# Optimization experiments

Hardware: AMD Instinct MI355X
Metric: run time of the kernel (lower is better)

The kernel has to match this reference:

```python
import jax, jax.numpy as jnp
import numpy as np

D_MODEL, D_K, D_V, H = 1024, 64, 64, 16
NEG_INF = -1e30  # finite stand-in for -inf masked_fill (grad-safe)


def setup_inputs() -> dict:
    key = jax.random.key(0)
    ks = jax.random.split(key, 16)
    b, nq, nk = 2, 1024, 1024
    def xavier(k, fan_in, fan_out):
        lim = np.sqrt(6.0 / (fan_in + fan_out)).astype(np.float32)
        return jax.random.uniform(k, (fan_in, fan_out), jnp.float32, -lim, lim)
    return {
        "queries": jax.random.normal(ks[0], (b, nq, D_MODEL), jnp.float32),
        "keys": jax.random.normal(ks[1], (b, nk, D_MODEL), jnp.float32),
        "values": jax.random.normal(ks[2], (b, nk, D_MODEL), jnp.float32),
        "attention_mask": jax.random.randint(ks[3], (b, H, nq, nk), 0, 2, jnp.int32),
        "attention_weights": jax.random.uniform(ks[4], (b, H, nq, nk), jnp.float32),
        "Wq": xavier(ks[5], D_MODEL, H * D_K), "bq": jnp.zeros((H * D_K,), jnp.float32),
        "Wk": xavier(ks[6], D_MODEL, H * D_K), "bk": jnp.zeros((H * D_K,), jnp.float32),
        "Wv": xavier(ks[7], D_MODEL, H * D_V), "bv": jnp.zeros((H * D_V,), jnp.float32),
        "Wo": xavier(ks[8], H * D_V, D_MODEL), "bo": jnp.zeros((D_MODEL,), jnp.float32),
    }


def reference(queries, keys, values, attention_mask, attention_weights,
              Wq, bq, Wk, bk, Wv, bv, Wo, bo):
    b, nq, _ = queries.shape
    nk = keys.shape[1]
    # project and split heads: [b, h, n, d]
    Q = (queries @ Wq + bq).reshape(b, nq, H, D_K).transpose(0, 2, 1, 3)
    K = (keys @ Wk + bk).reshape(b, nk, H, D_K).transpose(0, 2, 1, 3)
    V = (values @ Wv + bv).reshape(b, nk, H, D_V).transpose(0, 2, 1, 3)
    scale = jnp.asarray(1.0 / np.sqrt(D_K), queries.dtype)
    att = jnp.einsum('bhqd,bhkd->bhqk', Q, K) * scale
    att_map = att  # pre-weight/mask scores (torch .clone())
    att = att * attention_weights            # way='mul'
    att = jnp.where(attention_mask == 0, NEG_INF, att)
    att = jax.nn.softmax(att, axis=-1)
    out = jnp.einsum('bhqk,bhkd->bqhd', att, V).reshape(b, nq, H * D_V)
    out = out @ Wo + bo
    return out, att_map
```

## Files before the change

### kernel.cpp

```cpp
#include <hip/hip_runtime.h>

typedef _Float16 f16;
typedef __attribute__((ext_vector_type(4))) _Float16 half4;
typedef __attribute__((ext_vector_type(8))) _Float16 half8;
typedef __attribute__((ext_vector_type(4))) float v4f;
typedef __attribute__((ext_vector_type(4))) float f32x4v;
typedef __attribute__((ext_vector_type(4))) int i32x4;
typedef __attribute__((ext_vector_type(8))) unsigned short u16x8;

#define NEG_BIG -1e30f

#define MFMA32(a, b, c) __builtin_amdgcn_mfma_f32_16x16x32_f16(a, b, c, 0, 0, 0)
#if __has_builtin(__builtin_amdgcn_mfma_f32_16x16x16_f16)
#define MFMA16(a, b, c) __builtin_amdgcn_mfma_f32_16x16x16_f16(a, b, c, 0, 0, 0)
#else
#define MFMA16(a, b, c) __builtin_amdgcn_mfma_f32_16x16x16f16(a, b, c, 0, 0, 0)
#endif

__global__ __launch_bounds__(256) void cvt3_kernel(
    const float* __restrict__ q, const float* __restrict__ k, const float* __restrict__ v,
    f16* __restrict__ oq, f16* __restrict__ ok, f16* __restrict__ ov)
{
    int gid = blockIdx.x * 256 + threadIdx.x;
    int seg = gid >> 19;
    int off = (gid & 524287) << 2;
    const float* src = (seg == 0) ? q : (seg == 1) ? k : v;
    f16* dst = (seg == 0) ? oq : (seg == 1) ? ok : ov;
    f32x4v x = *(const f32x4v*)(src + off);
    union { f16 h[4]; unsigned long long u; } pk;
    pk.h[0] = (f16)x[0]; pk.h[1] = (f16)x[1]; pk.h[2] = (f16)x[2]; pk.h[3] = (f16)x[3];
    *(unsigned long long*)(dst + off) = pk.u;
}

__global__ __launch_bounds__(256) void wtrans_kernel(
    const float* __restrict__ w0, const float* __restrict__ w1,
    const float* __restrict__ w2, const float* __restrict__ w3,
    f16* __restrict__ o0, f16* __restrict__ o1, f16* __restrict__ o2, f16* __restrict__ o3)
{
    __shared__ f16 tile[64][72];
    int zs = blockIdx.z;
    const float* W = (zs == 0) ? w0 : (zs == 1) ? w1 : (zs == 2) ? w2 : w3;
    f16* O = (zs == 0) ? o0 : (zs == 1) ? o1 : (zs == 2) ? o2 : o3;
    int cx = blockIdx.x * 64;
    int ry = blockIdx.y * 64;
    int tid = threadIdx.x;
    #pragma unroll
    for (int p = 0; p < 4; ++p) {
        int idx = tid + p * 256;
        int r = idx >> 4, c4 = (idx & 15) << 2;
        f32x4v x = *(const f32x4v*)&W[(size_t)(ry + r) * 1024 + cx + c4];
        tile[r][c4 + 0] = (f16)x[0]; tile[r][c4 + 1] = (f16)x[1];
        tile[r][c4 + 2] = (f16)x[2]; tile[r][c4 + 3] = (f16)x[3];
    }
    __syncthreads();
    #pragma unroll
    for (int p = 0; p < 2; ++p) {
        int idx = tid + p * 256;
        int n = idx >> 3, c8 = (idx & 7) << 3;
        union { f16 h[8]; u16x8 u; } pk;
        #pragma unroll
        for (int j = 0; j < 8; ++j) pk.h[j] = tile[c8 + j][n];
        *(u16x8*)&O[(size_t)(cx + n) * 1024 + ry + c8] = pk.u;
    }
}

__device__ __forceinline__ void gemm_core(
    const f16* __restrict__ A, const f16* __restrict__ Bt,
    const float* __restrict__ bias, void* __restrict__ out, int mode)
{
    __shared__ f16 As[128 * 72];
    __shared__ f16 Bs[64 * 72];
    const int mbase = blockIdx.y * 128;
    const int nbase = blockIdx.x * 64;
    int tid = threadIdx.x;
    int lane = tid & 63, wave = tid >> 6;
    int ln = lane & 15, hi = lane >> 4;
    int wr = wave & 1, wc = wave >> 1;
    v4f acc[4][2];
    #pragma unroll
    for (int rt = 0; rt < 4; ++rt)
        #pragma unroll
        for (int ct = 0; ct < 2; ++ct) acc[rt][ct] = (v4f){0.f, 0.f, 0.f, 0.f};

    for (int kb = 0; kb < 1024; kb += 64) {
        __syncthreads();
        #pragma unroll
        for (int p = 0; p < 4; ++p) {
            int idx = tid + p * 256;
            int r = idx >> 3, c8 = (idx & 7) << 3;
            *(u16x8*)&As[r * 72 + c8] = *(const u16x8*)&A[(size_t)(mbase + r) * 1024 + kb + c8];
        }
        #pragma unroll
        for (int p = 0; p < 2; ++p) {
            int idx = tid + p * 256;
            int r = idx >> 3, c8 = (idx & 7) << 3;
            *(u16x8*)&Bs[r * 72 + c8] = *(const u16x8*)&Bt[(size_t)(nbase + r) * 1024 + kb + c8];
        }
        __syncthreads();
        #pragma unroll
        for (int kk = 0; kk < 64; kk += 32) {
            half8 aF[4], bF[2];
            #pragma unroll
            for (int rt = 0; rt < 4; ++rt)
                aF[rt] = *(const half8*)&As[(wr * 64 + rt * 16 + ln) * 72 + kk + 8 * hi];
            #pragma unroll
            for (int ct = 0; ct < 2; ++ct)
                bF[ct] = *(const half8*)&Bs[(wc * 32 + ct * 16 + ln) * 72 + kk + 8 * hi];
            #pragma unroll
            for (int rt = 0; rt < 4; ++rt)
                #pragma unroll
                for (int ct = 0; ct < 2; ++ct)
                    acc[rt][ct] = __builtin_amdgcn_mfma_f32_16x16x32_f16(aF[rt], bF[ct], acc[rt][ct], 0, 0, 0);
        }
    }
    #pragma unroll
    for (int rt = 0; rt < 4; ++rt)
      #pragma unroll
      for (int ct = 0; ct < 2; ++ct)
        #pragma unroll
        for (int r = 0; r < 4; ++r) {
            int m = mbase + wr * 64 + rt * 16 + hi * 4 + r;
            int n = nbase + wc * 32 + ct * 16 + ln;
            float val = acc[rt][ct][r] + bias[n];
            if (mode == 0) {
                int bb = m >> 10, nq = m & 1023, hh = n >> 6, d = n & 63;
                ((f16*)out)[(((size_t)(bb * 16 + hh)) * 1024 + nq) * 64 + d] = (f16)val;
            } else if (mode == 1) {
                int bb = m >> 10, nq = m & 1023, hh = n >> 6, d = n & 63;
                ((f16*)out)[(((size_t)(bb * 16 + hh)) * 64 + d) * 1024 + nq] = (f16)val;
            } else {
                ((float*)out)[(size_t)m * 1024 + n] = val;
            }
        }
}

__global__ __launch_bounds__(256) void qkv_gemm_kernel(
    const f16* __restrict__ xq, const f16* __restrict__ xk, const f16* __restrict__ xv,
    const f16* __restrict__ wqt, const f16* __restrict__ wkt, const f16* __restrict__ wvt,
    const float* __restrict__ bq, const float* __restrict__ bk, const float* __restrict__ bv,
    f16* __restrict__ oQ, f16* __restrict__ oK, f16* __restrict__ oVt)
{
    int z = blockIdx.z;
    const f16* A  = (z == 0) ? xq  : (z == 1) ? xk  : xv;
    const f16* B  = (z == 0) ? wqt : (z == 1) ? wkt : wvt;
    const float* bi = (z == 0) ? bq : (z == 1) ? bk : bv;
    void* out = (z == 0) ? (void*)oQ : (z == 1) ? (void*)oK : (void*)oVt;
    gemm_core(A, B, bi, out, (z == 2) ? 1 : 0);
}

__global__ __launch_bounds__(256) void o_gemm_kernel(
    const f16* __restrict__ A, const f16* __restrict__ Wot,
    const float* __restrict__ bo, float* __restrict__ out)
{
    gemm_core(A, Wot, bo, out, 2);
}

__global__ __launch_bounds__(512, 2) void attn_kernel(
    const f16* __restrict__ Qp, const f16* __restrict__ Kp, const f16* __restrict__ Vt,
    const float* __restrict__ weights, const int* __restrict__ mask,
    float* __restrict__ amap, float* __restrict__ Po, float* __restrict__ Ml)
{
    __shared__ f16 Ks[512 * 72];
    __shared__ f16 Vs[64 * 520];

    int h = blockIdx.x, qc = blockIdx.y, zid = blockIdx.z;
    int b = zid >> 1, kh = zid & 1;
    int bh = b * 16 + h;
    int tid = threadIdx.x;
    int lane = tid & 63, wave = tid >> 6;
    int ln = lane & 15, hi = lane >> 4;

    const f16* Kb = Kp + ((size_t)bh * 1024 + kh * 512) * 64;
    const f16* Vb = Vt + (size_t)bh * 64 * 1024 + kh * 512;

    #pragma unroll
    for (int i = 0; i < 8; ++i) {
        int c = tid + i * 512;
        int r = c >> 3, g = c & 7;
        *(u16x8*)&Ks[r * 72 + g * 8] = *(const u16x8*)&Kb[(size_t)c * 8];
    }
    #pragma unroll
    for (int i = 0; i < 8; ++i) {
        int c = tid + i * 512;
        int r = c >> 6, g = c & 63;
        *(u16x8*)&Vs[r * 520 + g * 8] = *(const u16x8*)&Vb[(size_t)r * 1024 + g * 8];
    }

    int qg = qc * 128 + wave * 16 + ln;
    const f16*  Qb = Qp + ((size_t)bh * 1024 + qg) * 64;
    const float* Wr = weights + ((size_t)bh * 1024 + qg) * 1024 + kh * 512;
    const int*   Mr = mask    + ((size_t)bh * 1024 + qg) * 1024 + kh * 512;
    float*       Ar = amap    + ((size_t)bh * 1024 + qg) * 1024 + kh * 512;

    half8 qf0 = *(const half8*)&Qb[8 * hi];
    half8 qf1 = *(const half8*)&Qb[32 + 8 * hi];

    float mrun = -3.0e38f, lrun = 0.f;
    v4f oacc[4];
    #pragma unroll
    for (int dt = 0; dt < 4; ++dt) oacc[dt] = (v4f){0.f, 0.f, 0.f, 0.f};

    f32x4v wA[4], wB[4]; i32x4 mA[4], mB[4];
    #pragma unroll
    for (int t = 0; t < 4; ++t) {
        wA[t] = *(const f32x4v*)&Wr[t * 16 + 4 * hi];
        mA[t] = *(const i32x4*)&Mr[t * 16 + 4 * hi];
        wB[t] = *(const f32x4v*)&Wr[64 + t * 16 + 4 * hi];
        mB[t] = *(const i32x4*)&Mr[64 + t * 16 + 4 * hi];
    }
    __syncthreads();

    auto process = [&](int kt, const f32x4v (&wb)[4], const i32x4 (&mb)[4]) {
        v4f st[4];
        #pragma unroll
        for (int t = 0; t < 4; ++t) {
            const f16* kr = &Ks[(kt * 64 + t * 16 + ln) * 72 + 8 * hi];
            half8 ka = *(const half8*)kr;
            half8 kc = *(const half8*)(kr + 32);
            v4f a = (v4f){0.f, 0.f, 0.f, 0.f};
            a = MFMA32(ka, qf0, a);
            a = MFMA32(kc, qf1, a);
            st[t] = a;
        }
        float z[4][4];
        #pragma unroll
        for (int t = 0; t < 4; ++t) {
            f32x4v sv = st[t] * 0.125f;
            __builtin_nontemporal_store(sv, (f32x4v*)&Ar[kt * 64 + t * 16 + 4 * hi]);
            #pragma unroll
            for (int r = 0; r < 4; ++r)
                z[t][r] = (mb[t][r] == 0) ? NEG_BIG : sv[r] * wb[t][r];
        }
        float tm = z[0][0];
        #pragma unroll
        for (int t = 0; t < 4; ++t)
            #pragma unroll
            for (int r = 0; r < 4; ++r) tm = fmaxf(tm, z[t][r]);
        tm = fmaxf(tm, __shfl_xor(tm, 16, 64));
        tm = fmaxf(tm, __shfl_xor(tm, 32, 64));
        float mnew = fmaxf(mrun, tm);
        float fsc = __expf(mrun - mnew);
        float p[4][4];
        float tsum = 0.f;
        #pragma unroll
        for (int t = 0; t < 4; ++t)
            #pragma unroll
            for (int r = 0; r < 4; ++r) { p[t][r] = __expf(z[t][r] - mnew); tsum += p[t][r]; }
        tsum += __shfl_xor(tsum, 16, 64);
        tsum += __shfl_xor(tsum, 32, 64);
        lrun = lrun * fsc + tsum;
        mrun = mnew;
        #pragma unroll
        for (int dt = 0; dt < 4; ++dt) oacc[dt] *= fsc;
        half4 pf[4];
        #pragma unroll
        for (int t = 0; t < 4; ++t) {
            half4 v;
            v[0] = (f16)p[t][0]; v[1] = (f16)p[t][1];
            v[2] = (f16)p[t][2]; v[3] = (f16)p[t][3];
            pf[t] = v;
        }
        #pragma unroll
        for (int t = 0; t < 4; ++t)
            #pragma unroll
            for (int dt = 0; dt < 4; ++dt) {
                half4 vf = *(const half4*)&Vs[(dt * 16 + ln) * 520 + kt * 64 + t * 16 + 4 * hi];
                oacc[dt] = MFMA16(vf, pf[t], oacc[dt]);
            }
    };

    #pragma unroll 1
    for (int kt2 = 0; kt2 < 4; ++kt2) {
        int kt = kt2 * 2;
        process(kt, wA, mA);
        if (kt2 < 3) {
            #pragma unroll
            for (int t = 0; t < 4; ++t) {
                wA[t] = *(const f32x4v*)&Wr[(kt + 2) * 64 + t * 16 + 4 * hi];
                mA[t] = *(const i32x4*)&Mr[(kt + 2) * 64 + t * 16 + 4 * hi];
            }
        }
        process(kt + 1, wB, mB);
        if (kt2 < 3) {
            #pragma unroll
            for (int t = 0; t < 4; ++t) {
                wB[t] = *(const f32x4v*)&Wr[(kt + 3) * 64 + t * 16 + 4 * hi];
                mB[t] = *(const i32x4*)&Mr[(kt + 3) * 64 + t * 16 + 4 * hi];
            }
        }
    }

    size_t prow = ((size_t)kh * 32 + bh) * 1024 + qg;
    #pragma unroll
    for (int dt = 0; dt < 4; ++dt)
        *(f32x4v*)&Po[prow * 64 + dt * 16 + 4 * hi] = oacc[dt];
    if (hi == 0) {
        float2 ml = make_float2(mrun, lrun);
        *(float2*)&Ml[prow * 2] = ml;
    }
}

__global__ __launch_bounds__(256) void merge_kernel(
    const float* __restrict__ Po, const float* __restrict__ Ml, f16* __restrict__ hout)
{
    int gid = blockIdx.x * 256 + threadIdx.x;
    int dq = gid & 15;
    int q  = (gid >> 4) & 1023;
    int bh = gid >> 14;
    int b = bh >> 4, h = bh & 15;
    size_t r0 = (size_t)bh * 1024 + q;
    size_t r1 = (size_t)(32 + bh) * 1024 + q;
    float2 ml0 = *(const float2*)&Ml[r0 * 2];
    float2 ml1 = *(const float2*)&Ml[r1 * 2];
    float M = fmaxf(ml0.x, ml1.x);
    float w0 = __expf(ml0.x - M), w1 = __expf(ml1.x - M);
    float rL = 1.0f / (w0 * ml0.y + w1 * ml1.y);
    f32x4v o0 = *(const f32x4v*)&Po[r0 * 64 + dq * 4];
    f32x4v o1 = *(const f32x4v*)&Po[r1 * 64 + dq * 4];
    half4 ov;
    #pragma unroll
    for (int j = 0; j < 4; ++j) ov[j] = (f16)((w0 * o0[j] + w1 * o1[j]) * rL);
    *(half4*)&hout[((size_t)(b * 1024 + q)) * 1024 + h * 64 + dq * 4] = ov;
}

extern "C" void kernel_launch(void* const* d_in, const int* in_sizes, int n_in,
                              void* d_out, int out_size, void* d_ws, size_t ws_size,
                              hipStream_t stream)
{
    const float* queries  = (const float*)d_in[0];
    const float* keys     = (const float*)d_in[1];
    const float* values   = (const float*)d_in[2];
    const int*   amask    = (const int*)d_in[3];
    const float* aweights = (const float*)d_in[4];
    const float* Wq = (const float*)d_in[5];  const float* bq = (const float*)d_in[6];
    const float* Wk = (const float*)d_in[7];  const float* bk = (const float*)d_in[8];
    const float* Wv = (const float*)d_in[9];  const float* bv = (const float*)d_in[10];
    const float* Wo = (const float*)d_in[11]; const float* bo = (const float*)d_in[12];

    char* ws = (char*)d_ws;
    const size_t MB = 1024 * 1024;
    f16* q_h  = (f16*)(ws + 0 * MB);
    f16* k_h  = (f16*)(ws + 4 * MB);
    f16* v_h  = (f16*)(ws + 8 * MB);
    f16* wqt  = (f16*)(ws + 12 * MB);
    f16* wkt  = (f16*)(ws + 14 * MB);
    f16* wvt  = (f16*)(ws + 16 * MB);
    f16* wot  = (f16*)(ws + 18 * MB);
    f16* Qp   = (f16*)(ws + 20 * MB);
    f16* Kp   = (f16*)(ws + 24 * MB);
    f16* Vt   = (f16*)(ws + 28 * MB);
    f16* hout = (f16*)(ws + 32 * MB);
    float* Po = (float*)(ws + 0 * MB);
    float* Ml = (float*)(ws + 16 * MB);

    float* out_main = (float*)d_out;
    float* att_map  = out_main + (size_t)2 * 1024 * 1024;

    cvt3_kernel<<<6144, 256, 0, stream>>>(queries, keys, values, q_h, k_h, v_h);
    wtrans_kernel<<<dim3(16, 16, 4), 256, 0, stream>>>(Wq, Wk, Wv, Wo, wqt, wkt, wvt, wot);
    qkv_gemm_kernel<<<dim3(16, 16, 3), 256, 0, stream>>>(q_h, k_h, v_h, wqt, wkt, wvt,
                                                         bq, bk, bv, Qp, Kp, Vt);
    attn_kernel<<<dim3(16, 8, 4), 512, 0, stream>>>(Qp, Kp, Vt, aweights, amask,
                                                    att_map, Po, Ml);
    merge_kernel<<<2048, 256, 0, stream>>>(Po, Ml, hout);
    o_gemm_kernel<<<dim3(16, 16, 1), 256, 0, stream>>>(hout, wot, bo, out_main);
}
```

Baseline: 160.6 us.

## Split attention keys into four chunks and store partial outputs in fp16

The attention kernel now splits the 1024 keys into four 256-key chunks instead of two halves. This doubles the grid to 1024 blocks, halves shared memory per block and raises the occupancy hint to 4 blocks per CU. Partial outputs are written as fp16 rather than fp32 to limit the extra workspace traffic, and the merge kernel combines four partials with log-sum-exp rescaling. The cost is more partial-result traffic and a larger merge, plus some precision loss from fp16 partials.

```diff
diff --git a/kernel.cpp b/kernel.cpp
--- a/kernel.cpp
+++ b/kernel.cpp
@@ -155,42 +155,42 @@
     gemm_core(A, Wot, bo, out, 2);
 }
 
-__global__ __launch_bounds__(512, 2) void attn_kernel(
+__global__ __launch_bounds__(512, 4) void attn_kernel(
     const f16* __restrict__ Qp, const f16* __restrict__ Kp, const f16* __restrict__ Vt,
     const float* __restrict__ weights, const int* __restrict__ mask,
-    float* __restrict__ amap, float* __restrict__ Po, float* __restrict__ Ml)
-{
-    __shared__ f16 Ks[512 * 72];
-    __shared__ f16 Vs[64 * 520];
+    float* __restrict__ amap, f16* __restrict__ Po, float* __restrict__ Ml)
+{
+    __shared__ f16 Ks[256 * 72];
+    __shared__ f16 Vs[64 * 264];
 
     int h = blockIdx.x, qc = blockIdx.y, zid = blockIdx.z;
-    int b = zid >> 1, kh = zid & 1;
+    int b = zid >> 2, kq = zid & 3;
     int bh = b * 16 + h;
     int tid = threadIdx.x;
     int lane = tid & 63, wave = tid >> 6;
     int ln = lane & 15, hi = lane >> 4;
 
-    const f16* Kb = Kp + ((size_t)bh * 1024 + kh * 512) * 64;
-    const f16* Vb = Vt + (size_t)bh * 64 * 1024 + kh * 512;
-
-    #pragma unroll
-    for (int i = 0; i < 8; ++i) {
+    const f16* Kb = Kp + ((size_t)bh * 1024 + kq * 256) * 64;
+    const f16* Vb = Vt + (size_t)bh * 64 * 1024 + kq * 256;
+
+    #pragma unroll
+    for (int i = 0; i < 4; ++i) {
         int c = tid + i * 512;
         int r = c >> 3, g = c & 7;
         *(u16x8*)&Ks[r * 72 + g * 8] = *(const u16x8*)&Kb[(size_t)c * 8];
     }
     #pragma unroll
-    for (int i = 0; i < 8; ++i) {
+    for (int i = 0; i < 4; ++i) {
         int c = tid + i * 512;
-        int r = c >> 6, g = c & 63;
-        *(u16x8*)&Vs[r * 520 + g * 8] = *(const u16x8*)&Vb[(size_t)r * 1024 + g * 8];
+        int r = c >> 5, g = c & 31;
+        *(u16x8*)&Vs[r * 264 + g * 8] = *(const u16x8*)&Vb[(size_t)r * 1024 + g * 8];
     }
 
     int qg = qc * 128 + wave * 16 + ln;
     const f16*  Qb = Qp + ((size_t)bh * 1024 + qg) * 64;
-    const float* Wr = weights + ((size_t)bh * 1024 + qg) * 1024 + kh * 512;
-    const int*   Mr = mask    + ((size_t)bh * 1024 + qg) * 1024 + kh * 512;
-    float*       Ar = amap    + ((size_t)bh * 1024 + qg) * 1024 + kh * 512;
+    const float* Wr = weights + ((size_t)bh * 1024 + qg) * 1024 + kq * 256;
+    const int*   Mr = mask    + ((size_t)bh * 1024 + qg) * 1024 + kq * 256;
+    float*       Ar = amap    + ((size_t)bh * 1024 + qg) * 1024 + kq * 256;
 
     half8 qf0 = *(const half8*)&Qb[8 * hi];
     half8 qf1 = *(const half8*)&Qb[32 + 8 * hi];
@@ -264,16 +264,16 @@
         for (int t = 0; t < 4; ++t)
             #pragma unroll
             for (int dt = 0; dt < 4; ++dt) {
-                half4 vf = *(const half4*)&Vs[(dt * 16 + ln) * 520 + kt * 64 + t * 16 + 4 * hi];
+                half4 vf = *(const half4*)&Vs[(dt * 16 + ln) * 264 + kt * 64 + t * 16 + 4 * hi];
                 oacc[dt] = MFMA16(vf, pf[t], oacc[dt]);
             }
     };
 
     #pragma unroll 1
-    for (int kt2 = 0; kt2 < 4; ++kt2) {
+    for (int kt2 = 0; kt2 < 2; ++kt2) {
         int kt = kt2 * 2;
         process(kt, wA, mA);
-        if (kt2 < 3) {
+        if (kt2 < 1) {
             #pragma unroll
             for (int t = 0; t < 4; ++t) {
                 wA[t] = *(const f32x4v*)&Wr[(kt + 2) * 64 + t * 16 + 4 * hi];
@@ -281,7 +281,7 @@
             }
         }
         process(kt + 1, wB, mB);
-        if (kt2 < 3) {
+        if (kt2 < 1) {
             #pragma unroll
             for (int t = 0; t < 4; ++t) {
                 wB[t] = *(const f32x4v*)&Wr[(kt + 3) * 64 + t * 16 + 4 * hi];
@@ -290,10 +290,14 @@
         }
     }
 
-    size_t prow = ((size_t)kh * 32 + bh) * 1024 + qg;
-    #pragma unroll
-    for (int dt = 0; dt < 4; ++dt)
-        *(f32x4v*)&Po[prow * 64 + dt * 16 + 4 * hi] = oacc[dt];
+    size_t prow = ((size_t)kq * 32 + bh) * 1024 + qg;
+    #pragma unroll
+    for (int dt = 0; dt < 4; ++dt) {
+        half4 ov;
+        #pragma unroll
+        for (int r = 0; r < 4; ++r) ov[r] = (f16)oacc[dt][r];
+        *(half4*)&Po[prow * 64 + dt * 16 + 4 * hi] = ov;
+    }
     if (hi == 0) {
         float2 ml = make_float2(mrun, lrun);
         *(float2*)&Ml[prow * 2] = ml;
@@ -301,25 +305,37 @@
 }
 
 __global__ __launch_bounds__(256) void merge_kernel(
-    const float* __restrict__ Po, const float* __restrict__ Ml, f16* __restrict__ hout)
+    const f16* __restrict__ Po, const float* __restrict__ Ml, f16* __restrict__ hout)
 {
     int gid = blockIdx.x * 256 + threadIdx.x;
     int dq = gid & 15;
     int q  = (gid >> 4) & 1023;
     int bh = gid >> 14;
     int b = bh >> 4, h = bh & 15;
-    size_t r0 = (size_t)bh * 1024 + q;
-    size_t r1 = (size_t)(32 + bh) * 1024 + q;
-    float2 ml0 = *(const float2*)&Ml[r0 * 2];
-    float2 ml1 = *(const float2*)&Ml[r1 * 2];
-    float M = fmaxf(ml0.x, ml1.x);
+    float2 ml0, ml1, ml2, ml3;
+    size_t r0 = ((size_t)0 * 32 + bh) * 1024 + q;
+    size_t r1 = ((size_t)1 * 32 + bh) * 1024 + q;
+    size_t r2 = ((size_t)2 * 32 + bh) * 1024 + q;
+    size_t r3 = ((size_t)3 * 32 + bh) * 1024 + q;
+    ml0 = *(const float2*)&Ml[r0 * 2];
+    ml1 = *(const float2*)&Ml[r1 * 2];
+    ml2 = *(const float2*)&Ml[r2 * 2];
+    ml3 = *(const float2*)&Ml[r3 * 2];
+    float M = fmaxf(fmaxf(ml0.x, ml1.x), fmaxf(ml2.x, ml3.x));
     float w0 = __expf(ml0.x - M), w1 = __expf(ml1.x - M);
-    float rL = 1.0f / (w0 * ml0.y + w1 * ml1.y);
-    f32x4v o0 = *(const f32x4v*)&Po[r0 * 64 + dq * 4];
-    f32x4v o1 = *(const f32x4v*)&Po[r1 * 64 + dq * 4];
+    float w2 = __expf(ml2.x - M), w3 = __expf(ml3.x - M);
+    float rL = 1.0f / (w0 * ml0.y + w1 * ml1.y + w2 * ml2.y + w3 * ml3.y);
+    half4 o0 = *(const half4*)&Po[r0 * 64 + dq * 4];
+    half4 o1 = *(const half4*)&Po[r1 * 64 + dq * 4];
+    half4 o2 = *(const half4*)&Po[r2 * 64 + dq * 4];
+    half4 o3 = *(const half4*)&Po[r3 * 64 + dq * 4];
     half4 ov;
     #pragma unroll
-    for (int j = 0; j < 4; ++j) ov[j] = (f16)((w0 * o0[j] + w1 * o1[j]) * rL);
+    for (int j = 0; j < 4; ++j) {
+        float acc = w0 * (float)o0[j] + w1 * (float)o1[j]
+                  + w2 * (float)o2[j] + w3 * (float)o3[j];
+        ov[j] = (f16)(acc * rL);
+    }
     *(half4*)&hout[((size_t)(b * 1024 + q)) * 1024 + h * 64 + dq * 4] = ov;
 }
 
@@ -350,7 +366,7 @@
     f16* Kp   = (f16*)(ws + 24 * MB);
     f16* Vt   = (f16*)(ws + 28 * MB);
     f16* hout = (f16*)(ws + 32 * MB);
-    float* Po = (float*)(ws + 0 * MB);
+    f16*   Po = (f16*)(ws + 0 * MB);
     float* Ml = (float*)(ws + 16 * MB);
 
     float* out_main = (float*)d_out;
@@ -360,7 +376,7 @@
     wtrans_kernel<<<dim3(16, 16, 4), 256, 0, stream>>>(Wq, Wk, Wv, Wo, wqt, wkt, wvt, wot);
     qkv_gemm_kernel<<<dim3(16, 16, 3), 256, 0, stream>>>(q_h, k_h, v_h, wqt, wkt, wvt,
                                                          bq, bk, bv, Qp, Kp, Vt);
-    attn_kernel<<<dim3(16, 8, 4), 512, 0, stream>>>(Qp, Kp, Vt, aweights, amask,
+    attn_kernel<<<dim3(16, 8, 8), 512, 0, stream>>>(Qp, Kp, Vt, aweights, amask,
                                                     att_map, Po, Ml);
     merge_kernel<<<2048, 256, 0, stream>>>(Po, Ml, hout);
     o_gemm_kernel<<<dim3(16, 16, 1), 256, 0, stream>>>(hout, wot, bo, out_main);
```

Result: slower. 179.6 us (+11.8%).

## Stream K/V tiles through double-buffered LDS with smaller attention blocks

Applied to the files above, without the earlier changes.

Rewrites the attention kernel so each 256-thread block covers 64 queries and streams 32-key K/V tiles through two small LDS buffers instead of staging the full 512-key half up front. This cuts LDS per block and doubles the grid, aiming for higher occupancy and overlap of global loads with compute. Partial outputs are stored in fp16 rather than fp32 to halve merge traffic. The cost is two barriers per tile, more K/V reloads across blocks, and lower precision on the partial accumulators.

```diff
diff --git a/kernel.cpp b/kernel.cpp
--- a/kernel.cpp
+++ b/kernel.cpp
@@ -155,13 +155,13 @@
     gemm_core(A, Wot, bo, out, 2);
 }
 
-__global__ __launch_bounds__(512, 2) void attn_kernel(
+__global__ __launch_bounds__(256) void attn_kernel(
     const f16* __restrict__ Qp, const f16* __restrict__ Kp, const f16* __restrict__ Vt,
     const float* __restrict__ weights, const int* __restrict__ mask,
-    float* __restrict__ amap, float* __restrict__ Po, float* __restrict__ Ml)
-{
-    __shared__ f16 Ks[512 * 72];
-    __shared__ f16 Vs[64 * 520];
+    float* __restrict__ amap, f16* __restrict__ Po, float* __restrict__ Ml)
+{
+    __shared__ f16 Ks[2][32 * 72];
+    __shared__ f16 Vs[2][64 * 40];
 
     int h = blockIdx.x, qc = blockIdx.y, zid = blockIdx.z;
     int b = zid >> 1, kh = zid & 1;
@@ -173,20 +173,10 @@
     const f16* Kb = Kp + ((size_t)bh * 1024 + kh * 512) * 64;
     const f16* Vb = Vt + (size_t)bh * 64 * 1024 + kh * 512;
 
-    #pragma unroll
-    for (int i = 0; i < 8; ++i) {
-        int c = tid + i * 512;
-        int r = c >> 3, g = c & 7;
-        *(u16x8*)&Ks[r * 72 + g * 8] = *(const u16x8*)&Kb[(size_t)c * 8];
-    }
-    #pragma unroll
-    for (int i = 0; i < 8; ++i) {
-        int c = tid + i * 512;
-        int r = c >> 6, g = c & 63;
-        *(u16x8*)&Vs[r * 520 + g * 8] = *(const u16x8*)&Vb[(size_t)r * 1024 + g * 8];
-    }
-
-    int qg = qc * 128 + wave * 16 + ln;
+    int krow = tid >> 3, kcol = (tid & 7) * 8;
+    int vrow = tid >> 2, vcol = (tid & 3) * 8;
+
+    int qg = qc * 64 + wave * 16 + ln;
     const f16*  Qb = Qp + ((size_t)bh * 1024 + qg) * 64;
     const float* Wr = weights + ((size_t)bh * 1024 + qg) * 1024 + kh * 512;
     const int*   Mr = mask    + ((size_t)bh * 1024 + qg) * 1024 + kh * 512;
@@ -195,26 +185,29 @@
     half8 qf0 = *(const half8*)&Qb[8 * hi];
     half8 qf1 = *(const half8*)&Qb[32 + 8 * hi];
 
+    *(half8*)&Ks[0][krow * 72 + kcol] = *(const half8*)&Kb[(size_t)krow * 64 + kcol];
+    *(half8*)&Vs[0][vrow * 40 + vcol] = *(const half8*)&Vb[(size_t)vrow * 1024 + vcol];
+
+    f32x4v wA[2], wB[2]; i32x4 mA[2], mB[2];
+    #pragma unroll
+    for (int t = 0; t < 2; ++t) {
+        wA[t] = *(const f32x4v*)&Wr[t * 16 + 4 * hi];
+        mA[t] = *(const i32x4*)&Mr[t * 16 + 4 * hi];
+        wB[t] = *(const f32x4v*)&Wr[32 + t * 16 + 4 * hi];
+        mB[t] = *(const i32x4*)&Mr[32 + t * 16 + 4 * hi];
+    }
+
     float mrun = -3.0e38f, lrun = 0.f;
     v4f oacc[4];
     #pragma unroll
     for (int dt = 0; dt < 4; ++dt) oacc[dt] = (v4f){0.f, 0.f, 0.f, 0.f};
-
-    f32x4v wA[4], wB[4]; i32x4 mA[4], mB[4];
-    #pragma unroll
-    for (int t = 0; t < 4; ++t) {
-        wA[t] = *(const f32x4v*)&Wr[t * 16 + 4 * hi];
-        mA[t] = *(const i32x4*)&Mr[t * 16 + 4 * hi];
-        wB[t] = *(const f32x4v*)&Wr[64 + t * 16 + 4 * hi];
-        mB[t] = *(const i32x4*)&Mr[64 + t * 16 + 4 * hi];
-    }
     __syncthreads();
 
-    auto process = [&](int kt, const f32x4v (&wb)[4], const i32x4 (&mb)[4]) {
-        v4f st[4];
-        #pragma unroll
-        for (int t = 0; t < 4; ++t) {
-            const f16* kr = &Ks[(kt * 64 + t * 16 + ln) * 72 + 8 * hi];
+    auto process = [&](int kt, int buf, const f32x4v (&wb)[2], const i32x4 (&mb)[2]) {
+        v4f st[2];
+        #pragma unroll
+        for (int t = 0; t < 2; ++t) {
+            const f16* kr = &Ks[buf][(t * 16 + ln) * 72 + 8 * hi];
             half8 ka = *(const half8*)kr;
             half8 kc = *(const half8*)(kr + 32);
             v4f a = (v4f){0.f, 0.f, 0.f, 0.f};
@@ -222,28 +215,28 @@
             a = MFMA32(kc, qf1, a);
             st[t] = a;
         }
-        float z[4][4];
-        #pragma unroll
-        for (int t = 0; t < 4; ++t) {
+        float z[2][4];
+        #pragma unroll
+        for (int t = 0; t < 2; ++t) {
             f32x4v sv = st[t] * 0.125f;
-            __builtin_nontemporal_store(sv, (f32x4v*)&Ar[kt * 64 + t * 16 + 4 * hi]);
+            __builtin_nontemporal_store(sv, (f32x4v*)&Ar[kt * 32 + t * 16 + 4 * hi]);
             #pragma unroll
             for (int r = 0; r < 4; ++r)
                 z[t][r] = (mb[t][r] == 0) ? NEG_BIG : sv[r] * wb[t][r];
         }
         float tm = z[0][0];
         #pragma unroll
-        for (int t = 0; t < 4; ++t)
+        for (int t = 0; t < 2; ++t)
             #pragma unroll
             for (int r = 0; r < 4; ++r) tm = fmaxf(tm, z[t][r]);
         tm = fmaxf(tm, __shfl_xor(tm, 16, 64));
         tm = fmaxf(tm, __shfl_xor(tm, 32, 64));
         float mnew = fmaxf(mrun, tm);
         float fsc = __expf(mrun - mnew);
-        float p[4][4];
+        float p[2][4];
         float tsum = 0.f;
         #pragma unroll
-        for (int t = 0; t < 4; ++t)
+        for (int t = 0; t < 2; ++t)
             #pragma unroll
             for (int r = 0; r < 4; ++r) { p[t][r] = __expf(z[t][r] - mnew); tsum += p[t][r]; }
         tsum += __shfl_xor(tsum, 16, 64);
@@ -252,48 +245,64 @@
         mrun = mnew;
         #pragma unroll
         for (int dt = 0; dt < 4; ++dt) oacc[dt] *= fsc;
-        half4 pf[4];
-        #pragma unroll
-        for (int t = 0; t < 4; ++t) {
+        half4 pf[2];
+        #pragma unroll
+        for (int t = 0; t < 2; ++t) {
             half4 v;
             v[0] = (f16)p[t][0]; v[1] = (f16)p[t][1];
             v[2] = (f16)p[t][2]; v[3] = (f16)p[t][3];
             pf[t] = v;
         }
         #pragma unroll
-        for (int t = 0; t < 4; ++t)
+        for (int t = 0; t < 2; ++t)
             #pragma unroll
             for (int dt = 0; dt < 4; ++dt) {
-                half4 vf = *(const half4*)&Vs[(dt * 16 + ln) * 520 + kt * 64 + t * 16 + 4 * hi];
+                half4 vf = *(const half4*)&Vs[buf][(dt * 16 + ln) * 40 + t * 16 + 4 * hi];
                 oacc[dt] = MFMA16(vf, pf[t], oacc[dt]);
             }
     };
 
     #pragma unroll 1
-    for (int kt2 = 0; kt2 < 4; ++kt2) {
-        int kt = kt2 * 2;
-        process(kt, wA, mA);
-        if (kt2 < 3) {
-            #pragma unroll
-            for (int t = 0; t < 4; ++t) {
-                wA[t] = *(const f32x4v*)&Wr[(kt + 2) * 64 + t * 16 + 4 * hi];
-                mA[t] = *(const i32x4*)&Mr[(kt + 2) * 64 + t * 16 + 4 * hi];
+    for (int kt = 0; kt < 16; ++kt) {
+        int buf = kt & 1;
+        half8 nk, nv;
+        if (kt < 15) {
+            nk = *(const half8*)&Kb[(size_t)((kt + 1) * 32 + krow) * 64 + kcol];
+            nv = *(const half8*)&Vb[(size_t)vrow * 1024 + (kt + 1) * 32 + vcol];
+        }
+        if (kt & 1) process(kt, buf, wB, mB);
+        else        process(kt, buf, wA, mA);
+        if (kt < 14) {
+            if (kt & 1) {
+                #pragma unroll
+                for (int t = 0; t < 2; ++t) {
+                    wB[t] = *(const f32x4v*)&Wr[(kt + 2) * 32 + t * 16 + 4 * hi];
+                    mB[t] = *(const i32x4*)&Mr[(kt + 2) * 32 + t * 16 + 4 * hi];
+                }
+            } else {
+                #pragma unroll
+                for (int t = 0; t < 2; ++t) {
+                    wA[t] = *(const f32x4v*)&Wr[(kt + 2) * 32 + t * 16 + 4 * hi];
+                    mA[t] = *(const i32x4*)&Mr[(kt + 2) * 32 + t * 16 + 4 * hi];
+                }
             }
         }
-        process(kt + 1, wB, mB);
-        if (kt2 < 3) {
-            #pragma unroll
-            for (int t = 0; t < 4; ++t) {
-                wB[t] = *(const f32x4v*)&Wr[(kt + 3) * 64 + t * 16 + 4 * hi];
-                mB[t] = *(const i32x4*)&Mr[(kt + 3) * 64 + t * 16 + 4 * hi];
-            }
+        if (kt < 15) {
+            __syncthreads();
+            *(half8*)&Ks[buf ^ 1][krow * 72 + kcol] = nk;
+            *(half8*)&Vs[buf ^ 1][vrow * 40 + vcol] = nv;
+            __syncthreads();
         }
     }
 
     size_t prow = ((size_t)kh * 32 + bh) * 1024 + qg;
     #pragma unroll
-    for (int dt = 0; dt < 4; ++dt)
-        *(f32x4v*)&Po[prow * 64 + dt * 16 + 4 * hi] = oacc[dt];
+    for (int dt = 0; dt < 4; ++dt) {
+        half4 ov;
+        #pragma unroll
+        for (int r = 0; r < 4; ++r) ov[r] = (f16)oacc[dt][r];
+        *(half4*)&Po[prow * 64 + dt * 16 + 4 * hi] = ov;
+    }
     if (hi == 0) {
         float2 ml = make_float2(mrun, lrun);
         *(float2*)&Ml[prow * 2] = ml;
@@ -301,7 +310,7 @@
 }
 
 __global__ __launch_bounds__(256) void merge_kernel(
-    const float* __restrict__ Po, const float* __restrict__ Ml, f16* __restrict__ hout)
+    const f16* __restrict__ Po, const float* __restrict__ Ml, f16* __restrict__ hout)
 {
     int gid = blockIdx.x * 256 + threadIdx.x;
     int dq = gid & 15;
@@ -315,11 +324,12 @@
     float M = fmaxf(ml0.x, ml1.x);
     float w0 = __expf(ml0.x - M), w1 = __expf(ml1.x - M);
     float rL = 1.0f / (w0 * ml0.y + w1 * ml1.y);
-    f32x4v o0 = *(const f32x4v*)&Po[r0 * 64 + dq * 4];
-    f32x4v o1 = *(const f32x4v*)&Po[r1 * 64 + dq * 4];
+    half4 o0 = *(const half4*)&Po[r0 * 64 + dq * 4];
+    half4 o1 = *(const half4*)&Po[r1 * 64 + dq * 4];
     half4 ov;
     #pragma unroll
-    for (int j = 0; j < 4; ++j) ov[j] = (f16)((w0 * o0[j] + w1 * o1[j]) * rL);
+    for (int j = 0; j < 4; ++j)
+        ov[j] = (f16)((w0 * (float)o0[j] + w1 * (float)o1[j]) * rL);
     *(half4*)&hout[((size_t)(b * 1024 + q)) * 1024 + h * 64 + dq * 4] = ov;
 }
 
@@ -350,7 +360,7 @@
     f16* Kp   = (f16*)(ws + 24 * MB);
     f16* Vt   = (f16*)(ws + 28 * MB);
     f16* hout = (f16*)(ws + 32 * MB);
-    float* Po = (float*)(ws + 0 * MB);
+    f16*   Po = (f16*)(ws + 0 * MB);
     float* Ml = (float*)(ws + 16 * MB);
 
     float* out_main = (float*)d_out;
@@ -360,8 +370,8 @@
     wtrans_kernel<<<dim3(16, 16, 4), 256, 0, stream>>>(Wq, Wk, Wv, Wo, wqt, wkt, wvt, wot);
     qkv_gemm_kernel<<<dim3(16, 16, 3), 256, 0, stream>>>(q_h, k_h, v_h, wqt, wkt, wvt,
                                                          bq, bk, bv, Qp, Kp, Vt);
-    attn_kernel<<<dim3(16, 8, 4), 512, 0, stream>>>(Qp, Kp, Vt, aweights, amask,
-                                                    att_map, Po, Ml);
+    attn_kernel<<<dim3(16, 16, 4), 256, 0, stream>>>(Qp, Kp, Vt, aweights, amask,
+                                                     att_map, Po, Ml);
     merge_kernel<<<2048, 256, 0, stream>>>(Po, Ml, hout);
     o_gemm_kernel<<<dim3(16, 16, 1), 256, 0, stream>>>(hout, wot, bo, out_main);
 }
```

Measured after the change: 175.6 us. 9.3% more time.

## Read V directly from global memory, drop V LDS tile, store partials in fp16

Applied to the files above, without the earlier changes.

The attention kernel no longer stages the V^T tile in shared memory. Each PV MFMA operand is now loaded straight from global or L2, which cuts LDS use per block and the staging cost. The two-occupancy launch bound is dropped, and the partial outputs Po are written as fp16 instead of fp32, halving merge traffic. The risks are strided 8-byte global loads of V inside the inner loop, higher latency there, and lower precision in the partial sums.

```diff
diff --git a/kernel.cpp b/kernel.cpp
--- a/kernel.cpp
+++ b/kernel.cpp
@@ -155,13 +155,12 @@
     gemm_core(A, Wot, bo, out, 2);
 }
 
-__global__ __launch_bounds__(512, 2) void attn_kernel(
+__global__ __launch_bounds__(512) void attn_kernel(
     const f16* __restrict__ Qp, const f16* __restrict__ Kp, const f16* __restrict__ Vt,
     const float* __restrict__ weights, const int* __restrict__ mask,
-    float* __restrict__ amap, float* __restrict__ Po, float* __restrict__ Ml)
+    float* __restrict__ amap, f16* __restrict__ Po, float* __restrict__ Ml)
 {
     __shared__ f16 Ks[512 * 72];
-    __shared__ f16 Vs[64 * 520];
 
     int h = blockIdx.x, qc = blockIdx.y, zid = blockIdx.z;
     int b = zid >> 1, kh = zid & 1;
@@ -177,13 +176,7 @@
     for (int i = 0; i < 8; ++i) {
         int c = tid + i * 512;
         int r = c >> 3, g = c & 7;
-        *(u16x8*)&Ks[r * 72 + g * 8] = *(const u16x8*)&Kb[(size_t)c * 8];
-    }
-    #pragma unroll
-    for (int i = 0; i < 8; ++i) {
-        int c = tid + i * 512;
-        int r = c >> 6, g = c & 63;
-        *(u16x8*)&Vs[r * 520 + g * 8] = *(const u16x8*)&Vb[(size_t)r * 1024 + g * 8];
+        *(half8*)&Ks[r * 72 + g * 8] = *(const half8*)&Kb[(size_t)c * 8];
     }
 
     int qg = qc * 128 + wave * 16 + ln;
@@ -261,12 +254,16 @@
             pf[t] = v;
         }
         #pragma unroll
-        for (int t = 0; t < 4; ++t)
-            #pragma unroll
-            for (int dt = 0; dt < 4; ++dt) {
-                half4 vf = *(const half4*)&Vs[(dt * 16 + ln) * 520 + kt * 64 + t * 16 + 4 * hi];
-                oacc[dt] = MFMA16(vf, pf[t], oacc[dt]);
-            }
+        for (int t = 0; t < 4; ++t) {
+            half4 vf0 = *(const half4*)&Vb[(size_t)(ln)       * 1024 + kt * 64 + t * 16 + 4 * hi];
+            half4 vf1 = *(const half4*)&Vb[(size_t)(16 + ln)  * 1024 + kt * 64 + t * 16 + 4 * hi];
+            half4 vf2 = *(const half4*)&Vb[(size_t)(32 + ln)  * 1024 + kt * 64 + t * 16 + 4 * hi];
+            half4 vf3 = *(const half4*)&Vb[(size_t)(48 + ln)  * 1024 + kt * 64 + t * 16 + 4 * hi];
+            oacc[0] = MFMA16(vf0, pf[t], oacc[0]);
+            oacc[1] = MFMA16(vf1, pf[t], oacc[1]);
+            oacc[2] = MFMA16(vf2, pf[t], oacc[2]);
+            oacc[3] = MFMA16(vf3, pf[t], oacc[3]);
+        }
     };
 
     #pragma unroll 1
@@ -292,8 +289,12 @@
 
     size_t prow = ((size_t)kh * 32 + bh) * 1024 + qg;
     #pragma unroll
-    for (int dt = 0; dt < 4; ++dt)
-        *(f32x4v*)&Po[prow * 64 + dt * 16 + 4 * hi] = oacc[dt];
+    for (int dt = 0; dt < 4; ++dt) {
+        half4 ov;
+        #pragma unroll
+        for (int r = 0; r < 4; ++r) ov[r] = (f16)oacc[dt][r];
+        *(half4*)&Po[prow * 64 + dt * 16 + 4 * hi] = ov;
+    }
     if (hi == 0) {
         float2 ml = make_float2(mrun, lrun);
         *(float2*)&Ml[prow * 2] = ml;
@@ -301,7 +302,7 @@
 }
 
 __global__ __launch_bounds__(256) void merge_kernel(
-    const float* __restrict__ Po, const float* __restrict__ Ml, f16* __restrict__ hout)
+    const f16* __restrict__ Po, const float* __restrict__ Ml, f16* __restrict__ hout)
 {
     int gid = blockIdx.x * 256 + threadIdx.x;
     int dq = gid & 15;
@@ -315,11 +316,12 @@
     float M = fmaxf(ml0.x, ml1.x);
     float w0 = __expf(ml0.x - M), w1 = __expf(ml1.x - M);
     float rL = 1.0f / (w0 * ml0.y + w1 * ml1.y);
-    f32x4v o0 = *(const f32x4v*)&Po[r0 * 64 + dq * 4];
-    f32x4v o1 = *(const f32x4v*)&Po[r1 * 64 + dq * 4];
+    half4 o0 = *(const half4*)&Po[r0 * 64 + dq * 4];
+    half4 o1 = *(const half4*)&Po[r1 * 64 + dq * 4];
     half4 ov;
     #pragma unroll
-    for (int j = 0; j < 4; ++j) ov[j] = (f16)((w0 * o0[j] + w1 * o1[j]) * rL);
+    for (int j = 0; j < 4; ++j)
+        ov[j] = (f16)((w0 * (float)o0[j] + w1 * (float)o1[j]) * rL);
     *(half4*)&hout[((size_t)(b * 1024 + q)) * 1024 + h * 64 + dq * 4] = ov;
 }
 
@@ -350,7 +352,7 @@
     f16* Kp   = (f16*)(ws + 24 * MB);
     f16* Vt   = (f16*)(ws + 28 * MB);
     f16* hout = (f16*)(ws + 32 * MB);
-    float* Po = (float*)(ws + 0 * MB);
+    f16*   Po = (f16*)(ws + 0 * MB);
     float* Ml = (float*)(ws + 16 * MB);
 
     float* out_main = (float*)d_out;
```

New measurement: 184.4 us. +14.8%, slower.
